# Kernel optimization log

Measured on AMD Instinct MI355X. Metric: run time of the kernel, lower is better.

The kernel has to match this reference:

```python
import jax, jax.numpy as jnp
import numpy as np

B, T = 8192, 2048
DT = 1.0


def setup_inputs() -> dict:
    key = jax.random.key(0)
    k1, k2, k3 = jax.random.split(key, 3)
    price = jax.random.normal(k1, (B, T), dtype=jnp.float32)
    hurst = jax.random.uniform(k2, (B, T), dtype=jnp.float32)
    vol_sigma = jax.random.uniform(k3, (B, T), dtype=jnp.float32)
    return {"price": price, "hurst": hurst, "vol_sigma": vol_sigma}


def _ekf(price, hurst, vol_sigma):
    dt = DT
    b = price.shape[0]
    dtype = price.dtype
    eye2 = jnp.eye(2, dtype=dtype)
    # initial state: [price_0, (price_1 - price_0)/dt]
    v0 = (price[:, 1] - price[:, 0]) / dt
    x0 = jnp.stack([price[:, 0], v0], axis=1)               # [B,2]
    P0 = jnp.broadcast_to(eye2, (b, 2, 2))                  # [B,2,2]

    e1 = jnp.array([1.0, 0.0], dtype=dtype)                 # H row = [1,0]

    def step(carry, inp):
        x, P = carry                                        # [B,2], [B,2,2]
        z, h, sig = inp                                     # each [B]
        rho = 0.5 + 0.5 * jax.nn.sigmoid(10.0 * (h - 0.5))
        a = dt * rho                                        # F[:,0,1]
        ones = jnp.ones_like(a)
        zeros = jnp.zeros_like(a)
        # F = [[1, a],[0, 1]] per batch element
        F = jnp.stack([jnp.stack([ones, a], -1),
                       jnp.stack([zeros, ones], -1)], axis=1)  # [B,2,2]
        scale = jnp.maximum(100.0 * sig, 1.0)               # clamp(min=1)
        # predict
        x_pred = jnp.einsum('bij,bj->bi', F, x)
        P_pred = jnp.einsum('bij,bjk,blk->bil', F, P, F) \
                 + (0.1 * scale)[:, None, None] * eye2      # + Q
        # update (H = [1,0] observes position only)
        y = z - x_pred[:, 0]                                # residual [B]
        S = P_pred[:, 0, 0] + scale                         # + R
        S_inv = 1.0 / (S + 1e-6)
        K = P_pred[:, :, 0] * S_inv[:, None]                # [B,2]
        x_new = x_pred + K * y[:, None]
        ImKH = eye2 - K[:, :, None] * e1[None, None, :]     # I - K H
        P_new = jnp.einsum('bij,bjk->bik', ImKH, P_pred)
        return (x_new, P_new), x_new

    xs = (price.T, hurst.T, vol_sigma.T)                    # [T,B] each
    _, states = jax.lax.scan(step, (x0, P0), xs)            # states: [T,B,2]
    return jnp.transpose(states, (1, 0, 2))                 # [B,T,2]


def reference(price, hurst, vol_sigma):
    return _ekf(price, hurst, vol_sigma)
```

## Files before the change

### kernel.cpp

```cpp
#include <hip/hip_runtime.h>


#define NB 8192
#define NT 2048
#define SEG 32
#define NC4 8

__device__ __forceinline__ float frcp(float x)  { return __builtin_amdgcn_rcpf(x); }
__device__ __forceinline__ float fexp2(float x) { return __builtin_amdgcn_exp2f(x); }

struct Elt {
    float A00, A01, A10, A11;
    float b0, b1;
    float C00, C01, C11;
    float e0, e1;
    float J00, J01, J11;
};

__device__ __forceinline__ Elt combine(const Elt& i, const Elt& j)
{
    float D00 = 1.0f + __builtin_fmaf(i.C00, j.J00, i.C01 * j.J01);
    float D01 =        __builtin_fmaf(i.C00, j.J01, i.C01 * j.J11);
    float D10 =        __builtin_fmaf(i.C01, j.J00, i.C11 * j.J01);
    float D11 = 1.0f + __builtin_fmaf(i.C01, j.J01, i.C11 * j.J11);
    float idet = frcp(__builtin_fmaf(D00, D11, -D01 * D10));
    float V00 =  D11 * idet, V01 = -D01 * idet;
    float V10 = -D10 * idet, V11 =  D00 * idet;
    float E00 = __builtin_fmaf(j.A00, V00, j.A01 * V10);
    float E01 = __builtin_fmaf(j.A00, V01, j.A01 * V11);
    float E10 = __builtin_fmaf(j.A10, V00, j.A11 * V10);
    float E11 = __builtin_fmaf(j.A10, V01, j.A11 * V11);
    Elt r;
    r.A00 = __builtin_fmaf(E00, i.A00, E01 * i.A10);
    r.A01 = __builtin_fmaf(E00, i.A01, E01 * i.A11);
    r.A10 = __builtin_fmaf(E10, i.A00, E11 * i.A10);
    r.A11 = __builtin_fmaf(E10, i.A01, E11 * i.A11);
    float t0 = i.b0 + __builtin_fmaf(i.C00, j.e0, i.C01 * j.e1);
    float t1 = i.b1 + __builtin_fmaf(i.C01, j.e0, i.C11 * j.e1);
    r.b0 = j.b0 + __builtin_fmaf(E00, t0, E01 * t1);
    r.b1 = j.b1 + __builtin_fmaf(E10, t0, E11 * t1);
    float T00 = __builtin_fmaf(E00, i.C00, E01 * i.C01);
    float T01 = __builtin_fmaf(E00, i.C01, E01 * i.C11);
    float T10 = __builtin_fmaf(E10, i.C00, E11 * i.C01);
    float T11 = __builtin_fmaf(E10, i.C01, E11 * i.C11);
    r.C00 = j.C00 + __builtin_fmaf(T00, j.A00, T01 * j.A01);
    r.C01 = j.C01 + __builtin_fmaf(T00, j.A10, T01 * j.A11);
    r.C11 = j.C11 + __builtin_fmaf(T10, j.A10, T11 * j.A11);
    float u0 = j.e0 - __builtin_fmaf(j.J00, i.b0, j.J01 * i.b1);
    float u1 = j.e1 - __builtin_fmaf(j.J01, i.b0, j.J11 * i.b1);
    float w0 = __builtin_fmaf(V00, u0, V10 * u1);
    float w1 = __builtin_fmaf(V01, u0, V11 * u1);
    r.e0 = i.e0 + __builtin_fmaf(i.A00, w0, i.A10 * w1);
    r.e1 = i.e1 + __builtin_fmaf(i.A01, w0, i.A11 * w1);
    float W00 = __builtin_fmaf(V00, j.J00, V10 * j.J01);
    float W01 = __builtin_fmaf(V00, j.J01, V10 * j.J11);
    float W10 = __builtin_fmaf(V01, j.J00, V11 * j.J01);
    float W11 = __builtin_fmaf(V01, j.J01, V11 * j.J11);
    float X00 = __builtin_fmaf(i.A00, W00, i.A10 * W10);
    float X01 = __builtin_fmaf(i.A00, W01, i.A10 * W11);
    float X10 = __builtin_fmaf(i.A01, W00, i.A11 * W10);
    float X11 = __builtin_fmaf(i.A01, W01, i.A11 * W11);
    r.J00 = i.J00 + __builtin_fmaf(X00, i.A00, X01 * i.A10);
    r.J01 = i.J01 + __builtin_fmaf(X00, i.A01, X01 * i.A11);
    r.J11 = i.J11 + __builtin_fmaf(X10, i.A01, X11 * i.A11);
    return r;
}

__device__ __forceinline__ void append_step(Elt& E, float z, float h, float sg,
                                            float& a_out, float& sc_out)
{
    float ee = fexp2(__builtin_fmaf(h, -14.4269504088896f, 7.2134752044448f));
    float a  = __builtin_fmaf(0.5f, frcp(1.0f + ee), 0.5f);
    float sc = fmaxf(100.0f * sg, 1.0f);
    float q  = 0.1f * sc;
    float r  = sc + 1e-6f;
    float Sinv = frcp(q + r);
    float u = q * Sinv;
    float v = r * Sinv;
    a_out = a; sc_out = sc;

    float cw0 = __builtin_fmaf(a, E.C01, E.C00);
    float cw1 = __builtin_fmaf(a, E.C11, E.C01);
    float g0 = Sinv * cw0, g1 = Sinv * cw1;
    float rho = frcp(__builtin_fmaf(a, g1, 1.0f + g0));
    float gp0 = rho * g0, gp1 = rho * g1;

    float s0 = __builtin_fmaf(a, E.A10, E.A00);
    float s1 = __builtin_fmaf(a, E.A11, E.A01);

    float wb0  = __builtin_fmaf(a, E.b1, E.b0);
    float beta = Sinv * (z - wb0);
    float bp0  = __builtin_fmaf(z, g0, E.b0);
    float bp1  = __builtin_fmaf(z, g1, E.b1);

    float N00 = __builtin_fmaf(-gp0, s0, E.A00);
    float N01 = __builtin_fmaf(-gp0, s1, E.A01);
    float N10 = __builtin_fmaf(-gp1, s0, E.A10);
    float N11 = __builtin_fmaf(-gp1, s1, E.A11);
    float A00n = v * __builtin_fmaf(a, N10, N00);
    float A01n = v * __builtin_fmaf(a, N11, N01);
    float wbp = __builtin_fmaf(a, bp1, bp0);
    float t0b = __builtin_fmaf(-gp0, wbp, bp0);
    float t1b = __builtin_fmaf(-gp1, wbp, bp1);
    float b0n = __builtin_fmaf(v, __builtin_fmaf(a, t1b, t0b), u * z);
    float M00 = __builtin_fmaf(-gp0, cw0, E.C00);
    float M01 = __builtin_fmaf(-gp0, cw1, E.C01);
    float M11 = __builtin_fmaf(-gp1, cw1, E.C11);
    float tc0 = __builtin_fmaf(a, M01, M00);
    float tc1 = __builtin_fmaf(a, M11, M01);
    float C00n = v * __builtin_fmaf(v, __builtin_fmaf(a, tc1, tc0), q);
    float C01n = v * tc1;
    float C11n = M11 + q;
    float br  = beta * rho;
    float e0n = __builtin_fmaf(br, s0, E.e0);
    float e1n = __builtin_fmaf(br, s1, E.e1);
    float kap = rho * Sinv;
    float ks0 = kap * s0, ks1 = kap * s1;
    float J00n = __builtin_fmaf(ks0, s0, E.J00);
    float J01n = __builtin_fmaf(ks0, s1, E.J01);
    float J11n = __builtin_fmaf(ks1, s1, E.J11);

    E.A00 = A00n; E.A01 = A01n; E.A10 = N10; E.A11 = N11;
    E.b0 = b0n;  E.b1 = t1b;
    E.C00 = C00n; E.C01 = C01n; E.C11 = C11n;
    E.e0 = e0n;  E.e1 = e1n;
    E.J00 = J00n; E.J01 = J01n; E.J11 = J11n;
}

__device__ __forceinline__ Elt shfl_up_elt(const Elt& x, int d)
{
    Elt r;
    r.A00 = __shfl_up(x.A00, d, 64); r.A01 = __shfl_up(x.A01, d, 64);
    r.A10 = __shfl_up(x.A10, d, 64); r.A11 = __shfl_up(x.A11, d, 64);
    r.b0  = __shfl_up(x.b0,  d, 64); r.b1  = __shfl_up(x.b1,  d, 64);
    r.C00 = __shfl_up(x.C00, d, 64); r.C01 = __shfl_up(x.C01, d, 64);
    r.C11 = __shfl_up(x.C11, d, 64);
    r.e0  = __shfl_up(x.e0,  d, 64); r.e1  = __shfl_up(x.e1,  d, 64);
    r.J00 = __shfl_up(x.J00, d, 64); r.J01 = __shfl_up(x.J01, d, 64);
    r.J11 = __shfl_up(x.J11, d, 64);
    return r;
}

__device__ __forceinline__ void replay_step(float z, float a, float sc,
        float& x0, float& x1, float& p00, float& p01, float& p11)
{
    float q  = 0.1f * sc;
    float rp = sc + 1e-6f;
    float qr = q + rp;
    float tA = __builtin_fmaf(a + a, p01, p00);
    float tB = __builtin_fmaf(a * a, p11, qr);
    float Seff = tA + tB;
    float Sinv = frcp(Seff);
    float pp00 = Seff - rp;
    float pp01 = __builtin_fmaf(a, p11, p01);
    float pp11 = p11 + q;
    float K0 = pp00 * Sinv, K1 = pp01 * Sinv;
    float xp0 = __builtin_fmaf(a, x1, x0);
    float y = z - xp0;
    x0 = __builtin_fmaf(K0, y, xp0);
    x1 = __builtin_fmaf(K1, y, x1);
    p00 = __builtin_fmaf(-K0, pp00, pp00);
    p01 = __builtin_fmaf(-K0, pp01, pp01);
    p11 = __builtin_fmaf(-K1, pp01, pp11);
}

__global__ __launch_bounds__(64)
void ekf_kernel(const float* __restrict__ price,
                const float* __restrict__ hurst,
                const float* __restrict__ sigv,
                float* __restrict__ out)
{
    __shared__ float2 as_lds[SEG][65];

    const int row  = blockIdx.x;
    const int lane = threadIdx.x;

    const float4* __restrict__ pr4 = (const float4*)(price + (size_t)row * NT) + lane * NC4;
    const float4* __restrict__ hu4 = (const float4*)(hurst + (size_t)row * NT) + lane * NC4;
    const float4* __restrict__ sg4 = (const float4*)(sigv  + (size_t)row * NT) + lane * NC4;

    float4 zb[NC4], hb[NC4], sb[NC4];
#pragma unroll
    for (int c = 0; c < NC4; ++c) zb[c] = pr4[c];
#pragma unroll
    for (int c = 0; c < NC4; ++c) hb[c] = hu4[c];
#pragma unroll
    for (int c = 0; c < NC4; ++c) sb[c] = sg4[c];

    const float z0l = zb[0].x, z1l = zb[0].y;

    Elt E;
    E.A00 = 1.0f; E.A01 = 0.0f; E.A10 = 0.0f; E.A11 = 1.0f;
    E.b0 = 0.0f; E.b1 = 0.0f;
    E.C00 = 0.0f; E.C01 = 0.0f; E.C11 = 0.0f;
    E.e0 = 0.0f; E.e1 = 0.0f;
    E.J00 = 0.0f; E.J01 = 0.0f; E.J11 = 0.0f;

#pragma unroll
    for (int c = 0; c < NC4; ++c) {
        float a0, c0, a1, c1, a2, c2, a3, c3;
        append_step(E, zb[c].x, hb[c].x, sb[c].x, a0, c0);
        append_step(E, zb[c].y, hb[c].y, sb[c].y, a1, c1);
        append_step(E, zb[c].z, hb[c].z, sb[c].z, a2, c2);
        append_step(E, zb[c].w, hb[c].w, sb[c].w, a3, c3);

        const int k = 4 * c;
        as_lds[k + 0][lane] = make_float2(a0, c0);
        as_lds[k + 1][lane] = make_float2(a1, c1);
        as_lds[k + 2][lane] = make_float2(a2, c2);
        as_lds[k + 3][lane] = make_float2(a3, c3);
    }

#pragma unroll
    for (int d = 1; d < 64; d <<= 1) {
        Elt o = shfl_up_elt(E, d);
        Elt c = combine(o, E);
        bool p = (lane >= d);
        E.A00 = p ? c.A00 : E.A00; E.A01 = p ? c.A01 : E.A01;
        E.A10 = p ? c.A10 : E.A10; E.A11 = p ? c.A11 : E.A11;
        E.b0  = p ? c.b0  : E.b0;  E.b1  = p ? c.b1  : E.b1;
        E.C00 = p ? c.C00 : E.C00; E.C01 = p ? c.C01 : E.C01;
        E.C11 = p ? c.C11 : E.C11;
        E.e0  = p ? c.e0  : E.e0;  E.e1  = p ? c.e1  : E.e1;
        E.J00 = p ? c.J00 : E.J00; E.J01 = p ? c.J01 : E.J01;
        E.J11 = p ? c.J11 : E.J11;
    }

    Elt ex = shfl_up_elt(E, 1);
    {
        bool l0 = (lane == 0);
        ex.A00 = l0 ? 1.0f : ex.A00; ex.A01 = l0 ? 0.0f : ex.A01;
        ex.A10 = l0 ? 0.0f : ex.A10; ex.A11 = l0 ? 1.0f : ex.A11;
        ex.b0  = l0 ? 0.0f : ex.b0;  ex.b1  = l0 ? 0.0f : ex.b1;
        ex.C00 = l0 ? 0.0f : ex.C00; ex.C01 = l0 ? 0.0f : ex.C01;
        ex.C11 = l0 ? 0.0f : ex.C11;
        ex.e0  = l0 ? 0.0f : ex.e0;  ex.e1  = l0 ? 0.0f : ex.e1;
        ex.J00 = l0 ? 0.0f : ex.J00; ex.J01 = l0 ? 0.0f : ex.J01;
        ex.J11 = l0 ? 0.0f : ex.J11;
    }

    float m00 = __shfl(z0l, 0, 64);
    float m01 = __shfl(z1l, 0, 64) - m00;

    float D00 = 1.0f + ex.J00, D01 = ex.J01, D11 = 1.0f + ex.J11;
    float idet = frcp(__builtin_fmaf(D00, D11, -D01 * D01));
    float V00 =  D11 * idet, V01 = -D01 * idet;
    float V10 = -D01 * idet, V11 =  D00 * idet;
    float E00 = __builtin_fmaf(ex.A00, V00, ex.A01 * V10);
    float E01 = __builtin_fmaf(ex.A00, V01, ex.A01 * V11);
    float E10 = __builtin_fmaf(ex.A10, V00, ex.A11 * V10);
    float E11 = __builtin_fmaf(ex.A10, V01, ex.A11 * V11);
    float t0 = m00 + ex.e0, t1 = m01 + ex.e1;
    float x0 = ex.b0 + __builtin_fmaf(E00, t0, E01 * t1);
    float x1 = ex.b1 + __builtin_fmaf(E10, t0, E11 * t1);
    float p00 = ex.C00 + __builtin_fmaf(E00, ex.A00, E01 * ex.A01);
    float p01 = ex.C01 + __builtin_fmaf(E00, ex.A10, E01 * ex.A11);
    float p11 = ex.C11 + __builtin_fmaf(E10, ex.A10, E11 * ex.A11);

#pragma unroll
    for (int c = 0; c < NC4; ++c) zb[c] = pr4[c];

#pragma unroll
    for (int c = 0; c < NC4; ++c) {
        const int k = 4 * c;
        float2 q0 = as_lds[k + 0][lane];
        float2 q1 = as_lds[k + 1][lane];
        float2 q2 = as_lds[k + 2][lane];
        float2 q3 = as_lds[k + 3][lane];

        replay_step(zb[c].x, q0.x, q0.y, x0, x1, p00, p01, p11);
        as_lds[k + 0][lane] = make_float2(x0, x1);
        replay_step(zb[c].y, q1.x, q1.y, x0, x1, p00, p01, p11);
        as_lds[k + 1][lane] = make_float2(x0, x1);
        replay_step(zb[c].z, q2.x, q2.y, x0, x1, p00, p01, p11);
        as_lds[k + 2][lane] = make_float2(x0, x1);
        replay_step(zb[c].w, q3.x, q3.y, x0, x1, p00, p01, p11);
        as_lds[k + 3][lane] = make_float2(x0, x1);
    }

    float2* __restrict__ op2 = (float2*)(out + (size_t)row * (size_t)NT * 2);
#pragma unroll
    for (int w = 0; w < 32; ++w) {
        int e = w * 64 + lane;
        op2[e] = as_lds[e & 31][e >> 5];
    }
}

extern "C" void kernel_launch(void* const* d_in, const int* in_sizes, int n_in,
                              void* d_out, int out_size, void* d_ws, size_t ws_size,
                              hipStream_t stream)
{
    const float* price = (const float*)d_in[0];
    const float* hurst = (const float*)d_in[1];
    const float* sigv  = (const float*)d_in[2];
    float* out = (float*)d_out;

    dim3 grid(NB), block(64);
    hipLaunchKernelGGL(ekf_kernel, grid, block, 0, stream, price, hurst, sigv, out);
}
```

Baseline: 289.7 us.

## Keep per-step coefficients in registers and store outputs directly as float4

Computes the (a, scale) coefficients once up front and keeps them in a 32-entry register array instead of writing them to LDS and reading them back in the replay pass. Outputs are collected in registers and written with per-lane float4 stores, so the LDS transpose staging is gone. Launch bounds add a minimum of 4 blocks per CU. Register pressure rises, which may cause spills. Each lane now writes its own contiguous 256-byte chunk, which makes the global stores less coalesced than the earlier lane-interleaved pattern.

```diff
diff --git a/kernel.cpp b/kernel.cpp
--- a/kernel.cpp
+++ b/kernel.cpp
@@ -66,18 +66,21 @@
     return r;
 }
 
-__device__ __forceinline__ void append_step(Elt& E, float z, float h, float sg,
-                                            float& a_out, float& sc_out)
+__device__ __forceinline__ float2 cvt_asc(float h, float sg)
 {
     float ee = fexp2(__builtin_fmaf(h, -14.4269504088896f, 7.2134752044448f));
     float a  = __builtin_fmaf(0.5f, frcp(1.0f + ee), 0.5f);
     float sc = fmaxf(100.0f * sg, 1.0f);
+    return make_float2(a, sc);
+}
+
+__device__ __forceinline__ void append_step(Elt& E, float z, float a, float sc)
+{
     float q  = 0.1f * sc;
     float r  = sc + 1e-6f;
     float Sinv = frcp(q + r);
     float u = q * Sinv;
     float v = r * Sinv;
-    a_out = a; sc_out = sc;
 
     float cw0 = __builtin_fmaf(a, E.C01, E.C00);
     float cw1 = __builtin_fmaf(a, E.C11, E.C01);
@@ -164,14 +167,12 @@
     p11 = __builtin_fmaf(-K1, pp01, pp11);
 }
 
-__global__ __launch_bounds__(64)
+__global__ __launch_bounds__(64, 4)
 void ekf_kernel(const float* __restrict__ price,
                 const float* __restrict__ hurst,
                 const float* __restrict__ sigv,
                 float* __restrict__ out)
 {
-    __shared__ float2 as_lds[SEG][65];
-
     const int row  = blockIdx.x;
     const int lane = threadIdx.x;
 
@@ -179,36 +180,41 @@
     const float4* __restrict__ hu4 = (const float4*)(hurst + (size_t)row * NT) + lane * NC4;
     const float4* __restrict__ sg4 = (const float4*)(sigv  + (size_t)row * NT) + lane * NC4;
 
-    float4 zb[NC4], hb[NC4], sb[NC4];
-#pragma unroll
-    for (int c = 0; c < NC4; ++c) zb[c] = pr4[c];
-#pragma unroll
-    for (int c = 0; c < NC4; ++c) hb[c] = hu4[c];
-#pragma unroll
-    for (int c = 0; c < NC4; ++c) sb[c] = sg4[c];
-
-    const float z0l = zb[0].x, z1l = zb[0].y;
-
+    float2 asc[SEG];
+    {
+        float4 hb[NC4], sb[NC4];
+#pragma unroll
+        for (int c = 0; c < NC4; ++c) hb[c] = hu4[c];
+#pragma unroll
+        for (int c = 0; c < NC4; ++c) sb[c] = sg4[c];
+#pragma unroll
+        for (int c = 0; c < NC4; ++c) {
+            asc[4 * c + 0] = cvt_asc(hb[c].x, sb[c].x);
+            asc[4 * c + 1] = cvt_asc(hb[c].y, sb[c].y);
+            asc[4 * c + 2] = cvt_asc(hb[c].z, sb[c].z);
+            asc[4 * c + 3] = cvt_asc(hb[c].w, sb[c].w);
+        }
+    }
+
+    float z0l, z1l;
     Elt E;
     E.A00 = 1.0f; E.A01 = 0.0f; E.A10 = 0.0f; E.A11 = 1.0f;
     E.b0 = 0.0f; E.b1 = 0.0f;
     E.C00 = 0.0f; E.C01 = 0.0f; E.C11 = 0.0f;
     E.e0 = 0.0f; E.e1 = 0.0f;
     E.J00 = 0.0f; E.J01 = 0.0f; E.J11 = 0.0f;
-
-#pragma unroll
-    for (int c = 0; c < NC4; ++c) {
-        float a0, c0, a1, c1, a2, c2, a3, c3;
-        append_step(E, zb[c].x, hb[c].x, sb[c].x, a0, c0);
-        append_step(E, zb[c].y, hb[c].y, sb[c].y, a1, c1);
-        append_step(E, zb[c].z, hb[c].z, sb[c].z, a2, c2);
-        append_step(E, zb[c].w, hb[c].w, sb[c].w, a3, c3);
-
-        const int k = 4 * c;
-        as_lds[k + 0][lane] = make_float2(a0, c0);
-        as_lds[k + 1][lane] = make_float2(a1, c1);
-        as_lds[k + 2][lane] = make_float2(a2, c2);
-        as_lds[k + 3][lane] = make_float2(a3, c3);
+    {
+        float4 zb[NC4];
+#pragma unroll
+        for (int c = 0; c < NC4; ++c) zb[c] = pr4[c];
+        z0l = zb[0].x; z1l = zb[0].y;
+#pragma unroll
+        for (int c = 0; c < NC4; ++c) {
+            append_step(E, zb[c].x, asc[4 * c + 0].x, asc[4 * c + 0].y);
+            append_step(E, zb[c].y, asc[4 * c + 1].x, asc[4 * c + 1].y);
+            append_step(E, zb[c].z, asc[4 * c + 2].x, asc[4 * c + 2].y);
+            append_step(E, zb[c].w, asc[4 * c + 3].x, asc[4 * c + 3].y);
+        }
     }
 
 #pragma unroll
@@ -257,33 +263,27 @@
     float p01 = ex.C01 + __builtin_fmaf(E00, ex.A10, E01 * ex.A11);
     float p11 = ex.C11 + __builtin_fmaf(E10, ex.A10, E11 * ex.A11);
 
-#pragma unroll
-    for (int c = 0; c < NC4; ++c) zb[c] = pr4[c];
-
-#pragma unroll
-    for (int c = 0; c < NC4; ++c) {
-        const int k = 4 * c;
-        float2 q0 = as_lds[k + 0][lane];
-        float2 q1 = as_lds[k + 1][lane];
-        float2 q2 = as_lds[k + 2][lane];
-        float2 q3 = as_lds[k + 3][lane];
-
-        replay_step(zb[c].x, q0.x, q0.y, x0, x1, p00, p01, p11);
-        as_lds[k + 0][lane] = make_float2(x0, x1);
-        replay_step(zb[c].y, q1.x, q1.y, x0, x1, p00, p01, p11);
-        as_lds[k + 1][lane] = make_float2(x0, x1);
-        replay_step(zb[c].z, q2.x, q2.y, x0, x1, p00, p01, p11);
-        as_lds[k + 2][lane] = make_float2(x0, x1);
-        replay_step(zb[c].w, q3.x, q3.y, x0, x1, p00, p01, p11);
-        as_lds[k + 3][lane] = make_float2(x0, x1);
-    }
-
-    float2* __restrict__ op2 = (float2*)(out + (size_t)row * (size_t)NT * 2);
-#pragma unroll
-    for (int w = 0; w < 32; ++w) {
-        int e = w * 64 + lane;
-        op2[e] = as_lds[e & 31][e >> 5];
-    }
+    float4 o[2 * NC4];
+    {
+        float4 zb[NC4];
+#pragma unroll
+        for (int c = 0; c < NC4; ++c) zb[c] = pr4[c];
+#pragma unroll
+        for (int c = 0; c < NC4; ++c) {
+            replay_step(zb[c].x, asc[4 * c + 0].x, asc[4 * c + 0].y, x0, x1, p00, p01, p11);
+            o[2 * c].x = x0; o[2 * c].y = x1;
+            replay_step(zb[c].y, asc[4 * c + 1].x, asc[4 * c + 1].y, x0, x1, p00, p01, p11);
+            o[2 * c].z = x0; o[2 * c].w = x1;
+            replay_step(zb[c].z, asc[4 * c + 2].x, asc[4 * c + 2].y, x0, x1, p00, p01, p11);
+            o[2 * c + 1].x = x0; o[2 * c + 1].y = x1;
+            replay_step(zb[c].w, asc[4 * c + 3].x, asc[4 * c + 3].y, x0, x1, p00, p01, p11);
+            o[2 * c + 1].z = x0; o[2 * c + 1].w = x1;
+        }
+    }
+
+    float4* __restrict__ op4 = (float4*)(out + (size_t)row * (size_t)NT * 2) + lane * (2 * NC4);
+#pragma unroll
+    for (int i = 0; i < 2 * NC4; ++i) op4[i] = o[i];
 }
 
 extern "C" void kernel_launch(void* const* d_in, const int* in_sizes, int n_in,
```

Result: slower. 418.2 us (+44.3%).

## Split each row across two waves with cross-wave scan carry via LDS

Applied to the files above, without the earlier changes.

Each row is now handled by a 128-thread block of two wavefronts instead of a single 64-lane wave, so every thread covers 16 timesteps rather than 32. Wave 0's scan total is written to LDS, and wave 1 combines it into its exclusive prefix. This halves the per-thread serial append and replay chain and register footprint. It adds a block-level barrier, an extra combine for the second wave, and twice as many threads per row.

```diff
diff --git a/kernel.cpp b/kernel.cpp
--- a/kernel.cpp
+++ b/kernel.cpp
@@ -3,8 +3,10 @@
 
 #define NB 8192
 #define NT 2048
-#define SEG 32
-#define NC4 8
+#define TPB 128
+#define SEG 16
+#define NC4 4
+#define LSTRIDE 130
 
 __device__ __forceinline__ float frcp(float x)  { return __builtin_amdgcn_rcpf(x); }
 __device__ __forceinline__ float fexp2(float x) { return __builtin_amdgcn_exp2f(x); }
@@ -164,30 +166,27 @@
     p11 = __builtin_fmaf(-K1, pp01, pp11);
 }
 
-__global__ __launch_bounds__(64)
+__global__ __launch_bounds__(TPB)
 void ekf_kernel(const float* __restrict__ price,
                 const float* __restrict__ hurst,
                 const float* __restrict__ sigv,
                 float* __restrict__ out)
 {
-    __shared__ float2 as_lds[SEG][65];
+    __shared__ float2 xlds[SEG][LSTRIDE];
+    __shared__ float  w0tot[14];
 
     const int row  = blockIdx.x;
-    const int lane = threadIdx.x;
-
-    const float4* __restrict__ pr4 = (const float4*)(price + (size_t)row * NT) + lane * NC4;
-    const float4* __restrict__ hu4 = (const float4*)(hurst + (size_t)row * NT) + lane * NC4;
-    const float4* __restrict__ sg4 = (const float4*)(sigv  + (size_t)row * NT) + lane * NC4;
-
-    float4 zb[NC4], hb[NC4], sb[NC4];
-#pragma unroll
-    for (int c = 0; c < NC4; ++c) zb[c] = pr4[c];
-#pragma unroll
-    for (int c = 0; c < NC4; ++c) hb[c] = hu4[c];
-#pragma unroll
-    for (int c = 0; c < NC4; ++c) sb[c] = sg4[c];
-
-    const float z0l = zb[0].x, z1l = zb[0].y;
+    const int tid  = threadIdx.x;
+    const int lane = tid & 63;
+    const int wav  = tid >> 6;
+
+    const float4* __restrict__ pr4 = (const float4*)(price + (size_t)row * NT) + tid * NC4;
+    const float4* __restrict__ hu4 = (const float4*)(hurst + (size_t)row * NT) + tid * NC4;
+    const float4* __restrict__ sg4 = (const float4*)(sigv  + (size_t)row * NT) + tid * NC4;
+
+    const float* __restrict__ prow = price + (size_t)row * NT;
+    const float m00 = prow[0];
+    const float m01 = prow[1] - m00;
 
     Elt E;
     E.A00 = 1.0f; E.A01 = 0.0f; E.A10 = 0.0f; E.A11 = 1.0f;
@@ -195,20 +194,28 @@
     E.C00 = 0.0f; E.C01 = 0.0f; E.C11 = 0.0f;
     E.e0 = 0.0f; E.e1 = 0.0f;
     E.J00 = 0.0f; E.J01 = 0.0f; E.J11 = 0.0f;
-
-#pragma unroll
-    for (int c = 0; c < NC4; ++c) {
-        float a0, c0, a1, c1, a2, c2, a3, c3;
-        append_step(E, zb[c].x, hb[c].x, sb[c].x, a0, c0);
-        append_step(E, zb[c].y, hb[c].y, sb[c].y, a1, c1);
-        append_step(E, zb[c].z, hb[c].z, sb[c].z, a2, c2);
-        append_step(E, zb[c].w, hb[c].w, sb[c].w, a3, c3);
-
-        const int k = 4 * c;
-        as_lds[k + 0][lane] = make_float2(a0, c0);
-        as_lds[k + 1][lane] = make_float2(a1, c1);
-        as_lds[k + 2][lane] = make_float2(a2, c2);
-        as_lds[k + 3][lane] = make_float2(a3, c3);
+    {
+        float4 zb[NC4], hb[NC4], sb[NC4];
+#pragma unroll
+        for (int c = 0; c < NC4; ++c) zb[c] = pr4[c];
+#pragma unroll
+        for (int c = 0; c < NC4; ++c) hb[c] = hu4[c];
+#pragma unroll
+        for (int c = 0; c < NC4; ++c) sb[c] = sg4[c];
+
+#pragma unroll
+        for (int c = 0; c < NC4; ++c) {
+            float a0, c0, a1, c1, a2, c2, a3, c3;
+            append_step(E, zb[c].x, hb[c].x, sb[c].x, a0, c0);
+            append_step(E, zb[c].y, hb[c].y, sb[c].y, a1, c1);
+            append_step(E, zb[c].z, hb[c].z, sb[c].z, a2, c2);
+            append_step(E, zb[c].w, hb[c].w, sb[c].w, a3, c3);
+            const int k = 4 * c;
+            xlds[k + 0][tid] = make_float2(a0, c0);
+            xlds[k + 1][tid] = make_float2(a1, c1);
+            xlds[k + 2][tid] = make_float2(a2, c2);
+            xlds[k + 3][tid] = make_float2(a3, c3);
+        }
     }
 
 #pragma unroll
@@ -226,6 +233,15 @@
         E.J11 = p ? c.J11 : E.J11;
     }
 
+    if (tid == 63) {
+        w0tot[0]  = E.A00; w0tot[1]  = E.A01; w0tot[2]  = E.A10; w0tot[3]  = E.A11;
+        w0tot[4]  = E.b0;  w0tot[5]  = E.b1;
+        w0tot[6]  = E.C00; w0tot[7]  = E.C01; w0tot[8]  = E.C11;
+        w0tot[9]  = E.e0;  w0tot[10] = E.e1;
+        w0tot[11] = E.J00; w0tot[12] = E.J01; w0tot[13] = E.J11;
+    }
+    __syncthreads();
+
     Elt ex = shfl_up_elt(E, 1);
     {
         bool l0 = (lane == 0);
@@ -238,9 +254,15 @@
         ex.J00 = l0 ? 0.0f : ex.J00; ex.J01 = l0 ? 0.0f : ex.J01;
         ex.J11 = l0 ? 0.0f : ex.J11;
     }
-
-    float m00 = __shfl(z0l, 0, 64);
-    float m01 = __shfl(z1l, 0, 64) - m00;
+    if (wav == 1) {
+        Elt w0;
+        w0.A00 = w0tot[0];  w0.A01 = w0tot[1];  w0.A10 = w0tot[2];  w0.A11 = w0tot[3];
+        w0.b0  = w0tot[4];  w0.b1  = w0tot[5];
+        w0.C00 = w0tot[6];  w0.C01 = w0tot[7];  w0.C11 = w0tot[8];
+        w0.e0  = w0tot[9];  w0.e1  = w0tot[10];
+        w0.J00 = w0tot[11]; w0.J01 = w0tot[12]; w0.J11 = w0tot[13];
+        ex = combine(w0, ex);
+    }
 
     float D00 = 1.0f + ex.J00, D01 = ex.J01, D11 = 1.0f + ex.J11;
     float idet = frcp(__builtin_fmaf(D00, D11, -D01 * D01));
@@ -257,32 +279,36 @@
     float p01 = ex.C01 + __builtin_fmaf(E00, ex.A10, E01 * ex.A11);
     float p11 = ex.C11 + __builtin_fmaf(E10, ex.A10, E11 * ex.A11);
 
-#pragma unroll
-    for (int c = 0; c < NC4; ++c) zb[c] = pr4[c];
-
-#pragma unroll
-    for (int c = 0; c < NC4; ++c) {
-        const int k = 4 * c;
-        float2 q0 = as_lds[k + 0][lane];
-        float2 q1 = as_lds[k + 1][lane];
-        float2 q2 = as_lds[k + 2][lane];
-        float2 q3 = as_lds[k + 3][lane];
-
-        replay_step(zb[c].x, q0.x, q0.y, x0, x1, p00, p01, p11);
-        as_lds[k + 0][lane] = make_float2(x0, x1);
-        replay_step(zb[c].y, q1.x, q1.y, x0, x1, p00, p01, p11);
-        as_lds[k + 1][lane] = make_float2(x0, x1);
-        replay_step(zb[c].z, q2.x, q2.y, x0, x1, p00, p01, p11);
-        as_lds[k + 2][lane] = make_float2(x0, x1);
-        replay_step(zb[c].w, q3.x, q3.y, x0, x1, p00, p01, p11);
-        as_lds[k + 3][lane] = make_float2(x0, x1);
-    }
+    {
+        float4 zb[NC4];
+#pragma unroll
+        for (int c = 0; c < NC4; ++c) zb[c] = pr4[c];
+
+#pragma unroll
+        for (int c = 0; c < NC4; ++c) {
+            const int k = 4 * c;
+            float2 q0 = xlds[k + 0][tid];
+            float2 q1 = xlds[k + 1][tid];
+            float2 q2 = xlds[k + 2][tid];
+            float2 q3 = xlds[k + 3][tid];
+
+            replay_step(zb[c].x, q0.x, q0.y, x0, x1, p00, p01, p11);
+            xlds[k + 0][tid] = make_float2(x0, x1);
+            replay_step(zb[c].y, q1.x, q1.y, x0, x1, p00, p01, p11);
+            xlds[k + 1][tid] = make_float2(x0, x1);
+            replay_step(zb[c].z, q2.x, q2.y, x0, x1, p00, p01, p11);
+            xlds[k + 2][tid] = make_float2(x0, x1);
+            replay_step(zb[c].w, q3.x, q3.y, x0, x1, p00, p01, p11);
+            xlds[k + 3][tid] = make_float2(x0, x1);
+        }
+    }
+    __syncthreads();
 
     float2* __restrict__ op2 = (float2*)(out + (size_t)row * (size_t)NT * 2);
 #pragma unroll
-    for (int w = 0; w < 32; ++w) {
-        int e = w * 64 + lane;
-        op2[e] = as_lds[e & 31][e >> 5];
+    for (int w = 0; w < SEG; ++w) {
+        int n = w * TPB + tid;
+        op2[n] = xlds[n & 15][n >> 4];
     }
 }
 
@@ -295,6 +321,6 @@
     const float* sigv  = (const float*)d_in[2];
     float* out = (float*)d_out;
 
-    dim3 grid(NB), block(64);
+    dim3 grid(NB), block(TPB);
     hipLaunchKernelGGL(ekf_kernel, grid, block, 0, stream, price, hurst, sigv, out);
 }
```

Result: faster. 278.0 us (-4.0%).
